# Performance work log

Hardware: AMD Instinct MI355X
Metric: run time of the kernel (lower is better)

## Reference

```python
import jax, jax.numpy as jnp
import numpy as np

B, V, E, C = 4, 150000, 450000, 62


def setup_inputs() -> dict:
    key = jax.random.key(0)
    k1, k2 = jax.random.split(key)
    vertex_tokens = jax.random.normal(k1, (B, V, C), dtype=jnp.float32)
    edges = jax.random.randint(k2, (B, E, 2), 0, V, dtype=jnp.int64)
    return {"vertex_tokens": vertex_tokens, "edges": edges}


def reference(vertex_tokens, edges):
    """vertices_to_edges: (B, V, C) -> (B, C, E).

    For each edge (v1, v2): edge_feat = (feat[v1] + feat[v2]) / 2,
    then permute to channels-first for MeshCNN.
    """
    # Batched endpoint gathers: [B, E, C] each
    v1_feat = jnp.take_along_axis(vertex_tokens, edges[:, :, 0][:, :, None], axis=1)
    v2_feat = jnp.take_along_axis(vertex_tokens, edges[:, :, 1][:, :, None], axis=1)
    edge_feat = (v1_feat + v2_feat) * 0.5  # [B, E, C]
    return jnp.transpose(edge_feat, (0, 2, 1))  # [B, C, E]
```

## Files before the change

kernel.cpp:

```cpp
#include <hip/hip_runtime.h>


constexpr int Bc = 4;
constexpr int Vc = 150000;
constexpr int Ec = 450000;
constexpr int Cc = 62;

__global__ __launch_bounds__(256) void v2e_kernel(
    const float* __restrict__ vt,
    const int*   __restrict__ edges,
    float*       __restrict__ out)
{
    const int e = blockIdx.x * 256 + threadIdx.x;
    const int b = blockIdx.y;
    if (e >= Ec) return;

    const int2 vv = *reinterpret_cast<const int2*>(edges + ((size_t)b * Ec + e) * 2);
    const float* __restrict__ r1 = vt + ((size_t)b * Vc + vv.x) * Cc;
    const float* __restrict__ r2 = vt + ((size_t)b * Vc + vv.y) * Cc;
    float* __restrict__ ob = out + (size_t)b * Cc * Ec + e;

#pragma unroll
    for (int c = 0; c < Cc; c += 2) {
        const float2 a = *reinterpret_cast<const float2*>(r1 + c);
        const float2 d = *reinterpret_cast<const float2*>(r2 + c);
        ob[(size_t)c       * Ec] = (a.x + d.x) * 0.5f;
        ob[(size_t)(c + 1) * Ec] = (a.y + d.y) * 0.5f;
    }
}

extern "C" void kernel_launch(void* const* d_in, const int* in_sizes, int n_in,
                              void* d_out, int out_size, void* d_ws, size_t ws_size,
                              hipStream_t stream) {
    const float* vt    = (const float*)d_in[0];
    const int*   edges = (const int*)d_in[1];
    float*       out   = (float*)d_out;

    dim3 grid((Ec + 255) / 256, Bc);
    v2e_kernel<<<grid, 256, 0, stream>>>(vt, edges, out);
}
```

Before: 816.8 us.

## Stage edge features in shared memory to coalesce gathers and transposed stores

Each block now handles 128 edges. Each wave gathers whole vertex rows, with the lanes indexed over channels, so reads within a row are contiguous. The averaged values go into a padded shared-memory tile, which is then written out channel-major with coalesced float2 stores. This replaces the per-thread strided reads and scattered per-channel stores of the old kernel, at the cost of shared memory, two barriers, and 2 of 64 lanes sitting idle during the gather.

```diff
diff --git a/kernel.cpp b/kernel.cpp
--- a/kernel.cpp
+++ b/kernel.cpp
@@ -5,27 +5,52 @@
 constexpr int Vc = 150000;
 constexpr int Ec = 450000;
 constexpr int Cc = 62;
+constexpr int TE = 128;
+constexpr int PITCH = TE + 2;
 
 __global__ __launch_bounds__(256) void v2e_kernel(
     const float* __restrict__ vt,
     const int*   __restrict__ edges,
     float*       __restrict__ out)
 {
-    const int e = blockIdx.x * 256 + threadIdx.x;
-    const int b = blockIdx.y;
-    if (e >= Ec) return;
+    __shared__ float tile[Cc * PITCH];
+    __shared__ int2  eidx[TE];
 
-    const int2 vv = *reinterpret_cast<const int2*>(edges + ((size_t)b * Ec + e) * 2);
-    const float* __restrict__ r1 = vt + ((size_t)b * Vc + vv.x) * Cc;
-    const float* __restrict__ r2 = vt + ((size_t)b * Vc + vv.y) * Cc;
-    float* __restrict__ ob = out + (size_t)b * Cc * Ec + e;
+    const int b  = blockIdx.y;
+    const int e0 = blockIdx.x * TE;
+    const int nE = min(TE, Ec - e0);
+    const int t    = threadIdx.x;
+    const int wave = t >> 6;
+    const int lane = t & 63;
 
-#pragma unroll
-    for (int c = 0; c < Cc; c += 2) {
-        const float2 a = *reinterpret_cast<const float2*>(r1 + c);
-        const float2 d = *reinterpret_cast<const float2*>(r2 + c);
-        ob[(size_t)c       * Ec] = (a.x + d.x) * 0.5f;
-        ob[(size_t)(c + 1) * Ec] = (a.y + d.y) * 0.5f;
+    if (t < nE)
+        eidx[t] = *reinterpret_cast<const int2*>(edges + ((size_t)b * Ec + e0 + t) * 2);
+    __syncthreads();
+
+    const float* __restrict__ vb = vt + (size_t)b * Vc * Cc;
+    const int iBeg = wave * 32;
+    const int iEnd = min(iBeg + 32, nE);
+#pragma unroll 4
+    for (int i = iBeg; i < iEnd; ++i) {
+        const int2 vv = eidx[i];
+        if (lane < Cc) {
+            const float a = vb[(size_t)vv.x * Cc + lane];
+            const float d = vb[(size_t)vv.y * Cc + lane];
+            tile[lane * PITCH + i] = (a + d) * 0.5f;
+        }
+    }
+    __syncthreads();
+
+    float* __restrict__ ob = out + (size_t)b * Cc * Ec + e0;
+    if (nE == TE) {
+        for (int c = wave; c < Cc; c += 4) {
+            const float2 v = *reinterpret_cast<const float2*>(&tile[c * PITCH + 2 * lane]);
+            *reinterpret_cast<float2*>(ob + (size_t)c * Ec + 2 * lane) = v;
+        }
+    } else {
+        for (int c = wave; c < Cc; c += 4)
+            for (int e = lane; e < nE; e += 64)
+                ob[(size_t)c * Ec + e] = tile[c * PITCH + e];
     }
 }
 
@@ -36,6 +61,6 @@
     const int*   edges = (const int*)d_in[1];
     float*       out   = (float*)d_out;
 
-    dim3 grid((Ec + 255) / 256, Bc);
+    dim3 grid((Ec + TE - 1) / TE, Bc);
     v2e_kernel<<<grid, 256, 0, stream>>>(vt, edges, out);
 }
```

After: 666.5 us. -18.4%, faster.
